# Optimization experiments

Measured on AMD Instinct MI355X. Metric: run time of the kernel, lower is better.

The kernel has to match this reference:

```python
import jax, jax.numpy as jnp
import numpy as np

B = 4096
M = 4            # n_modalities
T = 8            # n_tasks
D = 1024         # feature_dim per modality
DIN = D * M      # concat feature dim = 4096
H = 256          # hidden_dim
H2 = 2 * H       # 512
TEMP = 1.0
EPS = 1e-5


def _layernorm(x, g, b):
    # LayerNorm over last axis (torch nn.LayerNorm semantics, eps=1e-5)
    mu = jnp.mean(x, axis=-1, keepdims=True)
    var = jnp.mean(jnp.square(x - mu), axis=-1, keepdims=True)
    return (x - mu) * jax.lax.rsqrt(var + EPS) * g + b


def setup_inputs() -> dict:
    key = jax.random.key(0)
    ks = jax.random.split(key, 16)
    s = 0.02
    return {
        "f0": jax.random.normal(ks[0], (B, D), jnp.float32),
        "f1": jax.random.normal(ks[1], (B, D), jnp.float32),
        "f2": jax.random.normal(ks[2], (B, D), jnp.float32),
        "f3": jax.random.normal(ks[3], (B, D), jnp.float32),
        # per-task feature-net params (stacked ModuleList)
        "W1": jax.random.normal(ks[4], (T, DIN, H2), jnp.float32) * s,
        "b1": jnp.zeros((T, H2), jnp.float32),
        "g1": jnp.ones((T, H2), jnp.float32),
        "be1": jnp.zeros((T, H2), jnp.float32),
        "W2": jax.random.normal(ks[5], (T, H2, H), jnp.float32) * s,
        "b2": jnp.zeros((T, H), jnp.float32),
        "g2": jnp.ones((T, H), jnp.float32),
        "be2": jnp.zeros((T, H), jnp.float32),
        "task_emb": jax.random.normal(ks[6], (T, H), jnp.float32),
        # per-task weight-net params (Linear(2H -> M))
        "Ww": jax.random.normal(ks[7], (T, H2, M), jnp.float32) * s,
        "bw": jnp.zeros((T, M), jnp.float32),
        "task_ids": jax.random.randint(ks[8], (B,), 0, T, jnp.int32),
    }


def reference(f0, f1, f2, f3, W1, b1, g1, be1, W2, b2, g2, be2, task_emb, Ww, bw, task_ids):
    x = jnp.concatenate([f0, f1, f2, f3], axis=1)              # [B, DIN]
    # compute all-task feature nets densely (T is small), then gather per sample
    h = jnp.einsum('bd,tdh->bth', x, W1) + b1[None]            # [B, T, 2H]
    h = jax.nn.relu(_layernorm(h, g1[None], be1[None]))
    h = jnp.einsum('bth,thk->btk', h, W2) + b2[None]           # [B, T, H]
    h = jax.nn.relu(_layernorm(h, g2[None], be2[None]))
    hid = jnp.take_along_axis(h, task_ids[:, None, None], axis=1)[:, 0]  # [B, H]
    te = task_emb[task_ids]                                    # [B, H]
    comb = jnp.concatenate([hid, te], axis=1)                  # [B, 2H]
    # per-sample gather of small weight-net matrices (irregular access)
    raw = jnp.einsum('bh,bhm->bm', comb, Ww[task_ids]) + bw[task_ids]    # [B, M]
    return jax.nn.softmax(raw / TEMP, axis=1)
```

## Files before the change

kernel.cpp:

```cpp
#include <hip/hip_runtime.h>
#include <stdint.h>

#define B_N 4096
#define T_N 8
#define DIN 4096
#define H2C 512
#define HC 256
#define NWG1 1024
#define NWG2 264
#define SPLITK1 4

typedef __attribute__((ext_vector_type(8))) short bf16x8;
typedef __attribute__((ext_vector_type(4))) float f32x4;

static __device__ __forceinline__ unsigned short f2bf(float f) {
    union { float f; uint32_t u; } v; v.f = f;
    uint32_t u = v.u;
    uint32_t r = (u + 0x7FFFu + ((u >> 16) & 1u)) >> 16;
    return (unsigned short)r;
}

static __device__ __forceinline__ float bf2f(uint32_t h) {
    union { uint32_t u; float f; } v; v.u = h << 16; return v.f;
}

static __device__ __forceinline__ uint32_t pk2(float a, float b) {
    uint32_t r;
    asm volatile("v_cvt_pk_bf16_f32 %0, %1, %2" : "=v"(r) : "v"(a), "v"(b));
    return r;
}

static __device__ __forceinline__ void gl2lds16(const unsigned short* g, unsigned short* l) {
    __builtin_amdgcn_global_load_lds(
        (const __attribute__((address_space(1))) unsigned int*)(g),
        (__attribute__((address_space(3))) unsigned int*)(l), 16, 0, 0);
}

static __device__ __forceinline__ int xcd_remap(int bid, int nwg) {
    int xcd = bid & 7, idx = bid >> 3;
    int q = nwg >> 3, r = nwg & 7;
    return (xcd < r ? xcd * (q + 1) : r * (q + 1) + (xcd - r) * q) + idx;
}

__launch_bounds__(256)
__global__ void k_pre(const float* __restrict__ W1, const float* __restrict__ W2,
                      const int* __restrict__ task_ids,
                      const float* __restrict__ temb, const float* __restrict__ Ww,
                      const float* __restrict__ bw,
                      unsigned short* __restrict__ W1t, unsigned short* __restrict__ W2t,
                      int* __restrict__ order, int* __restrict__ tiles, int* __restrict__ bmap,
                      int* __restrict__ tiles2, int* __restrict__ ntile2,
                      float* __restrict__ tb) {
    int blk = blockIdx.x, tid = threadIdx.x;
    if (blk == 0) {
        __shared__ unsigned long long wtot[4][2];
        __shared__ int lc[T_N], lseg[T_N], tb1p[T_N + 1], tb2p[T_N + 1];
        int lane = tid & 63, wv = tid >> 6;
        int4 a0 = *(const int4*)(task_ids + tid * 16);
        int4 a1 = *(const int4*)(task_ids + tid * 16 + 4);
        int4 a2 = *(const int4*)(task_ids + tid * 16 + 8);
        int4 a3 = *(const int4*)(task_ids + tid * 16 + 12);
        int myt[16] = {a0.x, a0.y, a0.z, a0.w, a1.x, a1.y, a1.z, a1.w,
                       a2.x, a2.y, a2.z, a2.w, a3.x, a3.y, a3.z, a3.w};
        unsigned long long ph0 = 0, ph1 = 0;
        #pragma unroll
        for (int i = 0; i < 16; ++i) {
            int t = myt[i];
            if (t < 4) ph0 += 1ull << (t * 16); else ph1 += 1ull << ((t - 4) * 16);
        }
        unsigned long long s0 = ph0, s1 = ph1;
        for (int o = 1; o < 64; o <<= 1) {
            unsigned long long u0 = __shfl_up(s0, o);
            unsigned long long u1 = __shfl_up(s1, o);
            if (lane >= o) { s0 += u0; s1 += u1; }
        }
        if (lane == 63) { wtot[wv][0] = s0; wtot[wv][1] = s1; }
        __syncthreads();
        unsigned long long e0 = s0 - ph0, e1 = s1 - ph1;
        for (int w2 = 0; w2 < wv; ++w2) { e0 += wtot[w2][0]; e1 += wtot[w2][1]; }
        if (tid == 0) {
            unsigned long long t0 = 0, t1 = 0;
            for (int w2 = 0; w2 < 4; ++w2) { t0 += wtot[w2][0]; t1 += wtot[w2][1]; }
            int s = 0;
            for (int t = 0; t < T_N; ++t) {
                int c = (int)((t < 4 ? (t0 >> (t * 16)) : (t1 >> ((t - 4) * 16))) & 0xFFFF);
                lc[t] = c; lseg[t] = s; s += c;
            }
            int q1 = 0, q2 = 0;
            for (int t = 0; t < T_N; ++t) {
                tb1p[t] = q1; tb2p[t] = q2;
                q1 += (lc[t] + 127) >> 7; q2 += (lc[t] + 15) >> 4;
            }
            tb1p[T_N] = q1; tb2p[T_N] = q2;
            ntile2[0] = q2;
        }
        __syncthreads();
        unsigned long long r0 = e0, r1 = e1;
        #pragma unroll
        for (int i = 0; i < 16; ++i) {
            int t = myt[i], rk;
            if (t < 4) { rk = (int)((r0 >> (t * 16)) & 0xFFFF); r0 += 1ull << (t * 16); }
            else { int u = t - 4; rk = (int)((r1 >> (u * 16)) & 0xFFFF); r1 += 1ull << (u * 16); }
            order[lseg[t] + rk] = tid * 16 + i;
        }
        int n1 = tb1p[T_N], n2 = tb2p[T_N];
        for (int e = tid; e < n1; e += 256) {
            int t = 0; while (e >= tb1p[t + 1]) ++t;
            int rr = (e - tb1p[t]) << 7;
            tiles[3 * e] = t; tiles[3 * e + 1] = lseg[t] + rr;
            int rem = lc[t] - rr; tiles[3 * e + 2] = rem < 128 ? rem : 128;
        }
        for (int e = tid; e < n2; e += 256) {
            int t = 0; while (e >= tb2p[t + 1]) ++t;
            int rr = (e - tb2p[t]) << 4;
            tiles2[3 * e] = t; tiles2[3 * e + 1] = lseg[t] + rr;
            int rem = lc[t] - rr; tiles2[3 * e + 2] = rem < 16 ? rem : 16;
        }
        for (int s = tid; s < NWG1; s += 256) {
            int t = s & 7, j = s >> 3;
            int base = tb1p[t], nt = tb1p[t + 1] - base;
            bmap[s] = (j < nt * 16) ? (((base + (j >> 4)) << 4) | (j & 15)) : -1;
        }
        __syncthreads();
        if (tid == 0) {
            int freeslot = 0;
            for (int t = 0; t < T_N; ++t) {
                int base = tb1p[t], nt = tb1p[t + 1] - base;
                for (int j = 128; j < nt * 16; ++j) {
                    while (bmap[freeslot] >= 0) ++freeslot;
                    bmap[freeslot] = ((base + (j >> 4)) << 4) | (j & 15);
                }
            }
        }
        for (int t = wv; t < T_N; t += 4) {
            int m = lane & 3, hb = (lane >> 2) * 16;
            float s = 0.f;
            for (int h = 0; h < 16; ++h)
                s += temb[t * HC + hb + h] * Ww[((size_t)t * H2C + HC + hb + h) * 4 + m];
            for (int o = 4; o < 64; o <<= 1) s += __shfl_xor(s, o);
            if (lane < 4) tb[t * 4 + lane] = s + bw[t * 4 + lane];
        }
        return;
    }
    __shared__ float tile[64][65];
    const float* ip; unsigned short* op; int R, C, bx, by, t;
    if (blk < 4097) {
        int idx = blk - 1; bx = idx & 63; by = (idx >> 6) & 7; t = idx >> 9;
        R = DIN; C = H2C;
        ip = W1 + (size_t)t * R * C; op = W1t + (size_t)t * R * C;
    } else {
        int idx = blk - 4097; bx = idx & 7; by = (idx >> 3) & 3; t = idx >> 5;
        R = H2C; C = HC;
        ip = W2 + (size_t)t * R * C; op = W2t + (size_t)t * R * C;
    }
    int r0 = bx * 64, c0 = by * 64;
    int lr = tid >> 4, lc4 = (tid & 15) * 4;
    #pragma unroll
    for (int i = 0; i < 4; ++i) {
        float4 v = *(const float4*)&ip[(size_t)(r0 + lr + i * 16) * C + c0 + lc4];
        tile[lr + i * 16][lc4 + 0] = v.x;
        tile[lr + i * 16][lc4 + 1] = v.y;
        tile[lr + i * 16][lc4 + 2] = v.z;
        tile[lr + i * 16][lc4 + 3] = v.w;
    }
    __syncthreads();
    int r4 = (tid & 15) * 4;
    #pragma unroll
    for (int i = 0; i < 4; ++i) {
        int cc = i * 16 + (tid >> 4);
        uint2 wv;
        wv.x = (uint32_t)f2bf(tile[r4 + 0][cc]) | ((uint32_t)f2bf(tile[r4 + 1][cc]) << 16);
        wv.y = (uint32_t)f2bf(tile[r4 + 2][cc]) | ((uint32_t)f2bf(tile[r4 + 3][cc]) << 16);
        *(uint2*)&op[(size_t)(c0 + cc) * R + r0 + r4] = wv;
    }
}

__launch_bounds__(256)
__global__ void k_gemm1(const float* __restrict__ f0, const float* __restrict__ f1,
                        const float* __restrict__ f2, const float* __restrict__ f3,
                        const unsigned short* __restrict__ Bt,
                        unsigned short* __restrict__ Cb16, const int* __restrict__ order,
                        const int* __restrict__ tiles, const int* __restrict__ bmap) {
    int e = bmap[blockIdx.x];
    if (e < 0) return;
    int tix = e >> 4, sub = e & 15;
    int ct = sub >> 2, kc = sub & 3;
    int t = tiles[3 * tix], prow = tiles[3 * tix + 1], rows = tiles[3 * tix + 2];
    int kb = kc * (DIN / SPLITK1);
    const float* fsrc = (kc == 0) ? f0 : (kc == 1) ? f1 : (kc == 2) ? f2 : f3;

    __shared__ unsigned short lds[2][16384];

    int tid = threadIdx.x, lane = tid & 63, w = tid >> 6;
    int wm = w >> 1, wn = w & 1;

    const float* srcA[4];
    int ldsA[4];
    #pragma unroll
    for (int i = 0; i < 4; ++i) {
        int gi = i * 256 + tid;
        int row = gi >> 3, g = gi & 7;
        int rl = row < rows ? row : rows - 1;
        srcA[i] = fsrc + (size_t)order[prow + rl] * 1024 + g * 8;
        ldsA[i] = row * 64 + ((g ^ (row & 7)) * 8);
    }
    const unsigned short* pB[4];
    #pragma unroll
    for (int j = 0; j < 4; ++j) {
        int row = j * 32 + (tid >> 3);
        int colg = (tid & 7) ^ (row & 7);
        pB[j] = Bt + ((size_t)t * H2C + ct * 128 + row) * DIN + kb + colg * 8;
    }

    float4 a0[4], a1[4];
    auto loadA = [&](int k0) {
        #pragma unroll
        for (int i = 0; i < 4; ++i) {
            a0[i] = *(const float4*)(srcA[i] + k0);
            a1[i] = *(const float4*)(srcA[i] + k0 + 4);
        }
    };
    auto writeA = [&](int buf) {
        #pragma unroll
        for (int i = 0; i < 4; ++i) {
            uint4 wv;
            wv.x = pk2(a0[i].x, a0[i].y); wv.y = pk2(a0[i].z, a0[i].w);
            wv.z = pk2(a1[i].x, a1[i].y); wv.w = pk2(a1[i].z, a1[i].w);
            *(uint4*)&lds[buf][ldsA[i]] = wv;
        }
    };
    auto stageB = [&](int buf, int it) {
        unsigned short* dB = &lds[buf][8192 + w * 512];
        #pragma unroll
        for (int j = 0; j < 4; ++j) gl2lds16(pB[j] + it * 64, dB + j * 2048);
    };

    f32x4 acc[4][4];
    #pragma unroll
    for (int m = 0; m < 4; ++m)
        #pragma unroll
        for (int n = 0; n < 4; ++n)
            acc[m][n] = (f32x4){0.f, 0.f, 0.f, 0.f};

    constexpr int NIT = DIN / SPLITK1 / 64;
    loadA(0);
    stageB(0, 0);
    writeA(0);
    __syncthreads();
    int cur = 0;
    for (int it = 0; it < NIT; ++it) {
        if (it + 1 < NIT) {
            loadA((it + 1) * 64);
            stageB(cur ^ 1, it + 1);
            __builtin_amdgcn_sched_barrier(0);
        }
        const unsigned short* As = &lds[cur][0];
        const unsigned short* Bs = As + 8192;
        #pragma unroll
        for (int ks = 0; ks < 2; ++ks) {
            int g = ks * 4 + (lane >> 4);
            bf16x8 af[4], bfv[4];
            #pragma unroll
            for (int m = 0; m < 4; ++m) {
                int row = wm * 64 + m * 16 + (lane & 15);
                af[m] = *(const bf16x8*)&As[row * 64 + ((g ^ (row & 7)) * 8)];
            }
            #pragma unroll
            for (int n = 0; n < 4; ++n) {
                int row = wn * 64 + n * 16 + (lane & 15);
                bfv[n] = *(const bf16x8*)&Bs[row * 64 + ((g ^ (row & 7)) * 8)];
            }
            #pragma unroll
            for (int m = 0; m < 4; ++m)
                #pragma unroll
                for (int n = 0; n < 4; ++n)
                    acc[m][n] = __builtin_amdgcn_mfma_f32_16x16x32_bf16(af[m], bfv[n], acc[m][n], 0, 0, 0);
        }
        if (it + 1 < NIT) writeA(cur ^ 1);
        __syncthreads();
        cur ^= 1;
    }

    unsigned short* Cb = Cb16 + (size_t)kc * B_N * H2C;
    #pragma unroll
    for (int m = 0; m < 4; ++m) {
        #pragma unroll
        for (int n = 0; n < 4; ++n) {
            int col = ct * 128 + wn * 64 + n * 16 + (lane & 15);
            #pragma unroll
            for (int j = 0; j < 4; ++j) {
                int row = wm * 64 + m * 16 + (lane >> 4) * 4 + j;
                if (row < rows)
                    Cb[(size_t)(prow + row) * H2C + col] = f2bf(acc[m][n][j]);
            }
        }
    }
}

__launch_bounds__(256)
__global__ void k_gemm2f(const unsigned short* __restrict__ h1p, const unsigned short* __restrict__ W2t,
                         const float* __restrict__ b1, const float* __restrict__ g1,
                         const float* __restrict__ be1,
                         const float* __restrict__ b2, const float* __restrict__ g2,
                         const float* __restrict__ be2,
                         const float* __restrict__ Ww, const float* __restrict__ tb,
                         const int* __restrict__ order,
                         const int* __restrict__ tiles2, const int* __restrict__ ntile2,
                         float* __restrict__ out) {
    __shared__ unsigned short Asm[16 * 512];
    __shared__ unsigned short Bsm[2][256 * 32];
    __shared__ float red[16][4][4];

    int id = xcd_remap(blockIdx.x, NWG2);
    if (id >= ntile2[0]) return;
    int t = tiles2[3 * id], prow = tiles2[3 * id + 1], rows = tiles2[3 * id + 2];
    int tid = threadIdx.x, lane = tid & 63, w = tid >> 6;

    {
        int r = tid >> 4;
        int rl = r < rows ? r : rows - 1;
        int c0 = (tid & 15) * 32;
        const unsigned short* p0 = h1p + (size_t)(prow + rl) * H2C + c0;
        const float* pb = b1 + t * H2C + c0;
        float x[32];
        float s = 0.f, sq = 0.f;
        #pragma unroll
        for (int i = 0; i < 32; i += 8) {
            uint4 u0 = *(const uint4*)(p0 + i);
            uint4 u1 = *(const uint4*)(p0 + (size_t)B_N * H2C + i);
            uint4 u2 = *(const uint4*)(p0 + (size_t)2 * B_N * H2C + i);
            uint4 u3 = *(const uint4*)(p0 + (size_t)3 * B_N * H2C + i);
            uint32_t w0[4] = {u0.x, u0.y, u0.z, u0.w};
            uint32_t w1[4] = {u1.x, u1.y, u1.z, u1.w};
            uint32_t w2[4] = {u2.x, u2.y, u2.z, u2.w};
            uint32_t w3[4] = {u3.x, u3.y, u3.z, u3.w};
            float4 c0v = *(const float4*)(pb + i);
            float4 c1v = *(const float4*)(pb + i + 4);
            float cv[8] = {c0v.x, c0v.y, c0v.z, c0v.w, c1v.x, c1v.y, c1v.z, c1v.w};
            #pragma unroll
            for (int q = 0; q < 4; ++q) {
                float v0 = bf2f(w0[q] & 0xFFFFu) + bf2f(w1[q] & 0xFFFFu)
                         + bf2f(w2[q] & 0xFFFFu) + bf2f(w3[q] & 0xFFFFu) + cv[2 * q];
                float v1 = bf2f(w0[q] >> 16) + bf2f(w1[q] >> 16)
                         + bf2f(w2[q] >> 16) + bf2f(w3[q] >> 16) + cv[2 * q + 1];
                x[i + 2 * q] = v0; x[i + 2 * q + 1] = v1;
                s += v0 + v1; sq += v0 * v0 + v1 * v1;
            }
        }
        #pragma unroll
        for (int o = 1; o < 16; o <<= 1) { s += __shfl_xor(s, o); sq += __shfl_xor(sq, o); }
        float mean = s * (1.f / H2C);
        float var = sq * (1.f / H2C) - mean * mean;
        float rstd = rsqrtf(var + 1e-5f);
        const float* pg = g1 + t * H2C + c0;
        const float* pe = be1 + t * H2C + c0;
        #pragma unroll
        for (int i = 0; i < 32; i += 8) {
            unsigned short y[8];
            #pragma unroll
            for (int q = 0; q < 8; q += 4) {
                float4 gv = *(const float4*)(pg + i + q);
                float4 ev = *(const float4*)(pe + i + q);
                y[q + 0] = f2bf(fmaxf((x[i + q + 0] - mean) * rstd * gv.x + ev.x, 0.f));
                y[q + 1] = f2bf(fmaxf((x[i + q + 1] - mean) * rstd * gv.y + ev.y, 0.f));
                y[q + 2] = f2bf(fmaxf((x[i + q + 2] - mean) * rstd * gv.z + ev.z, 0.f));
                y[q + 3] = f2bf(fmaxf((x[i + q + 3] - mean) * rstd * gv.w + ev.w, 0.f));
            }
            uint4 wv;
            wv.x = (uint32_t)y[0] | ((uint32_t)y[1] << 16);
            wv.y = (uint32_t)y[2] | ((uint32_t)y[3] << 16);
            wv.z = (uint32_t)y[4] | ((uint32_t)y[5] << 16);
            wv.w = (uint32_t)y[6] | ((uint32_t)y[7] << 16);
            int g = (c0 + i) >> 3;
            *(uint4*)&Asm[r * 512 + ((g ^ (r & 7)) * 8)] = wv;
        }
    }

    auto stageB = [&](int buf, int it) {
        #pragma unroll
        for (int j = 0; j < 4; ++j) {
            int G = j * 256 + tid;
            int row = G >> 2, g = G & 3;
            int colg = g ^ (row & 3);
            gl2lds16(W2t + ((size_t)t * HC + row) * H2C + it * 32 + colg * 8,
                     &Bsm[buf][(j * 256 + w * 64) * 8]);
        }
    };

    stageB(0, 0);
    __syncthreads();

    f32x4 acc[4];
    #pragma unroll
    for (int n = 0; n < 4; ++n) acc[n] = (f32x4){0.f, 0.f, 0.f, 0.f};

    for (int it = 0; it < 16; ++it) {
        if (it + 1 < 16) stageB((it + 1) & 1, it + 1);
        const unsigned short* Bs = &Bsm[it & 1][0];
        int g = lane >> 4;
        int arow = lane & 15;
        bf16x8 af = *(const bf16x8*)&Asm[arow * 512 + (((it * 4 + g) ^ (arow & 7)) * 8)];
        #pragma unroll
        for (int n = 0; n < 4; ++n) {
            int brow = w * 64 + n * 16 + arow;
            bf16x8 bv = *(const bf16x8*)&Bs[brow * 32 + ((g ^ (brow & 3)) * 8)];
            acc[n] = __builtin_amdgcn_mfma_f32_16x16x32_bf16(af, bv, acc[n], 0, 0, 0);
        }
        __syncthreads();
    }

    float b2v[4], g2v[4], e2v[4];
    float4 wv[4];
    #pragma unroll
    for (int n = 0; n < 4; ++n) {
        int col = w * 64 + n * 16 + (lane & 15);
        b2v[n] = b2[t * HC + col];
        g2v[n] = g2[t * HC + col];
        e2v[n] = be2[t * HC + col];
        wv[n] = *(const float4*)&Ww[((size_t)t * H2C + col) * 4];
    }
    float s4[4], q4[4];
    #pragma unroll
    for (int j = 0; j < 4; ++j) {
        float s = 0.f, sq = 0.f;
        #pragma unroll
        for (int n = 0; n < 4; ++n) {
            float xv = acc[n][j] + b2v[n];
            s += xv; sq += xv * xv;
        }
        #pragma unroll
        for (int o = 1; o < 16; o <<= 1) { s += __shfl_xor(s, o); sq += __shfl_xor(sq, o); }
        s4[j] = s; q4[j] = sq;
    }
    if ((lane & 15) == 0) {
        #pragma unroll
        for (int j = 0; j < 4; ++j) {
            int r = (lane >> 4) * 4 + j;
            red[r][w][0] = s4[j];
            red[r][w][1] = q4[j];
        }
    }
    __syncthreads();
    float mean[4], rstd[4];
    #pragma unroll
    for (int j = 0; j < 4; ++j) {
        int r = (lane >> 4) * 4 + j;
        float S = red[r][0][0] + red[r][1][0] + red[r][2][0] + red[r][3][0];
        float SQ = red[r][0][1] + red[r][1][1] + red[r][2][1] + red[r][3][1];
        mean[j] = S * (1.f / HC);
        float var = SQ * (1.f / HC) - mean[j] * mean[j];
        rstd[j] = rsqrtf(var + 1e-5f);
    }
    float p[4][4];
    #pragma unroll
    for (int j = 0; j < 4; ++j) {
        p[j][0] = 0.f; p[j][1] = 0.f; p[j][2] = 0.f; p[j][3] = 0.f;
        #pragma unroll
        for (int n = 0; n < 4; ++n) {
            float yv = fmaxf((acc[n][j] + b2v[n] - mean[j]) * rstd[j] * g2v[n] + e2v[n], 0.f);
            p[j][0] += yv * wv[n].x; p[j][1] += yv * wv[n].y;
            p[j][2] += yv * wv[n].z; p[j][3] += yv * wv[n].w;
        }
        #pragma unroll
        for (int m = 0; m < 4; ++m)
            #pragma unroll
            for (int o = 1; o < 16; o <<= 1) p[j][m] += __shfl_xor(p[j][m], o);
    }
    __syncthreads();
    if ((lane & 15) == 0) {
        #pragma unroll
        for (int j = 0; j < 4; ++j) {
            int r = (lane >> 4) * 4 + j;
            red[r][w][0] = p[j][0]; red[r][w][1] = p[j][1];
            red[r][w][2] = p[j][2]; red[r][w][3] = p[j][3];
        }
    }
    __syncthreads();
    if (tid < 16 && tid < rows) {
        float raw[4];
        #pragma unroll
        for (int m = 0; m < 4; ++m)
            raw[m] = red[tid][0][m] + red[tid][1][m] + red[tid][2][m] + red[tid][3][m] + tb[t * 4 + m];
        float mx = fmaxf(fmaxf(raw[0], raw[1]), fmaxf(raw[2], raw[3]));
        float e0 = expf(raw[0] - mx), e1 = expf(raw[1] - mx);
        float e2 = expf(raw[2] - mx), e3 = expf(raw[3] - mx);
        float si = 1.f / (e0 + e1 + e2 + e3);
        *(float4*)(out + (size_t)order[prow + tid] * 4) = make_float4(e0 * si, e1 * si, e2 * si, e3 * si);
    }
}

extern "C" void kernel_launch(void* const* d_in, const int* in_sizes, int n_in,
                              void* d_out, int out_size, void* d_ws, size_t ws_size,
                              hipStream_t stream) {
    const float* f0 = (const float*)d_in[0];
    const float* f1 = (const float*)d_in[1];
    const float* f2 = (const float*)d_in[2];
    const float* f3 = (const float*)d_in[3];
    const float* W1 = (const float*)d_in[4];
    const float* b1 = (const float*)d_in[5];
    const float* g1 = (const float*)d_in[6];
    const float* be1 = (const float*)d_in[7];
    const float* W2 = (const float*)d_in[8];
    const float* b2 = (const float*)d_in[9];
    const float* g2 = (const float*)d_in[10];
    const float* be2 = (const float*)d_in[11];
    const float* temb = (const float*)d_in[12];
    const float* Ww = (const float*)d_in[13];
    const float* bw = (const float*)d_in[14];
    const int* task_ids = (const int*)d_in[15];
    float* out = (float*)d_out;

    char* ws = (char*)d_ws;
    size_t off = 0;
    auto walloc = [&](size_t bytes) -> void* {
        void* p = ws + off;
        off = (off + bytes + 255) & ~(size_t)255;
        return p;
    };
    float* tb = (float*)walloc(128);
    int* tiles = (int*)walloc(64 * 3 * 4);
    int* bmap = (int*)walloc(NWG1 * 4);
    int* tiles2 = (int*)walloc(272 * 3 * 4);
    int* ntile2 = (int*)walloc(4);
    int* order = (int*)walloc((size_t)B_N * 4);
    unsigned short* W1t = (unsigned short*)walloc((size_t)T_N * H2C * DIN * 2);
    unsigned short* W2t = (unsigned short*)walloc((size_t)T_N * HC * H2C * 2);
    unsigned short* h1p = (unsigned short*)walloc((size_t)SPLITK1 * B_N * H2C * 2);

    k_pre<<<4353, 256, 0, stream>>>(W1, W2, task_ids, temb, Ww, bw,
                                    W1t, W2t, order, tiles, bmap, tiles2, ntile2, tb);
    k_gemm1<<<NWG1, 256, 0, stream>>>(f0, f1, f2, f3, W1t, h1p, order, tiles, bmap);
    k_gemm2f<<<NWG2, 256, 0, stream>>>(h1p, W2t, b1, g1, be1, b2, g2, be2, Ww, tb,
                                       order, tiles2, ntile2, out);
}
```

Measured before the change: 81.88 us.

## Stage fp32 activations directly to LDS via global_load_lds and convert at fragment load

In the first GEMM, the A operand (fp32 features) is no longer loaded into registers, converted to bf16 and written to LDS. It is now copied asynchronously into LDS as fp32 with global_load_lds and converted to bf16 when each MFMA fragment is read. The K step per iteration is halved from 64 to 32, and the B tile uses a new XOR swizzle to match. This removes the register round-trip and VGPR pressure of the A path. In exchange it doubles A's LDS footprint per element, adds conversion work inside the MFMA loop, and doubles the number of barriers.

```diff
diff --git a/kernel.cpp b/kernel.cpp
--- a/kernel.cpp
+++ b/kernel.cpp
@@ -31,6 +31,12 @@
 }
 
 static __device__ __forceinline__ void gl2lds16(const unsigned short* g, unsigned short* l) {
+    __builtin_amdgcn_global_load_lds(
+        (const __attribute__((address_space(1))) unsigned int*)(g),
+        (__attribute__((address_space(3))) unsigned int*)(l), 16, 0, 0);
+}
+
+static __device__ __forceinline__ void gl2lds16f(const float* g, float* l) {
     __builtin_amdgcn_global_load_lds(
         (const __attribute__((address_space(1))) unsigned int*)(g),
         (__attribute__((address_space(3))) unsigned int*)(l), 16, 0, 0);
@@ -189,50 +195,35 @@
     int kb = kc * (DIN / SPLITK1);
     const float* fsrc = (kc == 0) ? f0 : (kc == 1) ? f1 : (kc == 2) ? f2 : f3;
 
-    __shared__ unsigned short lds[2][16384];
+    __shared__ float ldsA[2][128 * 32];
+    __shared__ unsigned short ldsB[2][128 * 32];
 
     int tid = threadIdx.x, lane = tid & 63, w = tid >> 6;
     int wm = w >> 1, wn = w & 1;
 
-    const float* srcA[4];
-    int ldsA[4];
-    #pragma unroll
-    for (int i = 0; i < 4; ++i) {
-        int gi = i * 256 + tid;
-        int row = gi >> 3, g = gi & 7;
+    const float* pA4[4];
+    #pragma unroll
+    for (int j = 0; j < 4; ++j) {
+        int slot = j * 256 + tid;
+        int row = slot >> 3, gd = slot & 7;
         int rl = row < rows ? row : rows - 1;
-        srcA[i] = fsrc + (size_t)order[prow + rl] * 1024 + g * 8;
-        ldsA[i] = row * 64 + ((g ^ (row & 7)) * 8);
-    }
-    const unsigned short* pB[4];
-    #pragma unroll
-    for (int j = 0; j < 4; ++j) {
-        int row = j * 32 + (tid >> 3);
-        int colg = (tid & 7) ^ (row & 7);
-        pB[j] = Bt + ((size_t)t * H2C + ct * 128 + row) * DIN + kb + colg * 8;
-    }
-
-    float4 a0[4], a1[4];
-    auto loadA = [&](int k0) {
-        #pragma unroll
-        for (int i = 0; i < 4; ++i) {
-            a0[i] = *(const float4*)(srcA[i] + k0);
-            a1[i] = *(const float4*)(srcA[i] + k0 + 4);
-        }
-    };
-    auto writeA = [&](int buf) {
-        #pragma unroll
-        for (int i = 0; i < 4; ++i) {
-            uint4 wv;
-            wv.x = pk2(a0[i].x, a0[i].y); wv.y = pk2(a0[i].z, a0[i].w);
-            wv.z = pk2(a1[i].x, a1[i].y); wv.w = pk2(a1[i].z, a1[i].w);
-            *(uint4*)&lds[buf][ldsA[i]] = wv;
-        }
-    };
-    auto stageB = [&](int buf, int it) {
-        unsigned short* dB = &lds[buf][8192 + w * 512];
-        #pragma unroll
-        for (int j = 0; j < 4; ++j) gl2lds16(pB[j] + it * 64, dB + j * 2048);
+        pA4[j] = fsrc + (size_t)order[prow + rl] * 1024 + (gd ^ (row & 7)) * 4;
+    }
+    const unsigned short* pB[2];
+    #pragma unroll
+    for (int j = 0; j < 2; ++j) {
+        int slot = j * 256 + tid;
+        int row = slot >> 2, gd = slot & 3;
+        pB[j] = Bt + ((size_t)t * H2C + ct * 128 + row) * DIN + kb + (gd ^ ((row >> 1) & 3)) * 8;
+    }
+
+    auto stage = [&](int buf, int it) {
+        float* dA = &ldsA[buf][(size_t)w * 256];
+        unsigned short* dB = &ldsB[buf][(size_t)w * 512];
+        #pragma unroll
+        for (int j = 0; j < 4; ++j) gl2lds16f(pA4[j] + it * 32, dA + j * 1024);
+        #pragma unroll
+        for (int j = 0; j < 2; ++j) gl2lds16(pB[j] + it * 32, dB + j * 2048);
     };
 
     f32x4 acc[4][4];
@@ -242,41 +233,36 @@
         for (int n = 0; n < 4; ++n)
             acc[m][n] = (f32x4){0.f, 0.f, 0.f, 0.f};
 
-    constexpr int NIT = DIN / SPLITK1 / 64;
-    loadA(0);
-    stageB(0, 0);
-    writeA(0);
+    constexpr int NIT = (DIN / SPLITK1) / 32;
+    stage(0, 0);
     __syncthreads();
     int cur = 0;
+    int g = lane >> 4, lrow = lane & 15;
     for (int it = 0; it < NIT; ++it) {
-        if (it + 1 < NIT) {
-            loadA((it + 1) * 64);
-            stageB(cur ^ 1, it + 1);
-            __builtin_amdgcn_sched_barrier(0);
-        }
-        const unsigned short* As = &lds[cur][0];
-        const unsigned short* Bs = As + 8192;
-        #pragma unroll
-        for (int ks = 0; ks < 2; ++ks) {
-            int g = ks * 4 + (lane >> 4);
-            bf16x8 af[4], bfv[4];
+        if (it + 1 < NIT) stage(cur ^ 1, it + 1);
+        const float* Af = &ldsA[cur][0];
+        const unsigned short* Bs = &ldsB[cur][0];
+        bf16x8 af[4], bfv[4];
+        #pragma unroll
+        for (int m = 0; m < 4; ++m) {
+            int row = wm * 64 + m * 16 + lrow;
+            float4 lo = *(const float4*)(Af + row * 32 + (((2 * g) ^ (row & 7)) * 4));
+            float4 hi = *(const float4*)(Af + row * 32 + (((2 * g + 1) ^ (row & 7)) * 4));
+            union { uint4 u; bf16x8 b; } cv;
+            cv.u.x = pk2(lo.x, lo.y); cv.u.y = pk2(lo.z, lo.w);
+            cv.u.z = pk2(hi.x, hi.y); cv.u.w = pk2(hi.z, hi.w);
+            af[m] = cv.b;
+        }
+        #pragma unroll
+        for (int n = 0; n < 4; ++n) {
+            int row = wn * 64 + n * 16 + lrow;
+            bfv[n] = *(const bf16x8*)&Bs[row * 32 + ((g ^ ((row >> 1) & 3)) * 8)];
+        }
+        #pragma unroll
+        for (int m = 0; m < 4; ++m)
             #pragma unroll
-            for (int m = 0; m < 4; ++m) {
-                int row = wm * 64 + m * 16 + (lane & 15);
-                af[m] = *(const bf16x8*)&As[row * 64 + ((g ^ (row & 7)) * 8)];
-            }
-            #pragma unroll
-            for (int n = 0; n < 4; ++n) {
-                int row = wn * 64 + n * 16 + (lane & 15);
-                bfv[n] = *(const bf16x8*)&Bs[row * 64 + ((g ^ (row & 7)) * 8)];
-            }
-            #pragma unroll
-            for (int m = 0; m < 4; ++m)
-                #pragma unroll
-                for (int n = 0; n < 4; ++n)
-                    acc[m][n] = __builtin_amdgcn_mfma_f32_16x16x32_bf16(af[m], bfv[n], acc[m][n], 0, 0, 0);
-        }
-        if (it + 1 < NIT) writeA(cur ^ 1);
+            for (int n = 0; n < 4; ++n)
+                acc[m][n] = __builtin_amdgcn_mfma_f32_16x16x32_bf16(af[m], bfv[n], acc[m][n], 0, 0, 0);
         __syncthreads();
         cur ^= 1;
     }
```

After: 85.04 us. +3.9%, slower.

## Deepen A-operand prefetch to two stages with explicit vmcnt waits

Applied to the files above, without the earlier changes.

Adds a second register set for the fp32 A tile so global loads are issued two iterations ahead instead of one. Replaces __syncthreads with hand-placed s_waitcnt vmcnt/lgkmcnt counts plus s_barrier, so outstanding B direct-to-LDS loads and A loads can overlap the MFMA work. This hides more global memory latency at the cost of extra VGPRs (32 more floats per thread), which may lower occupancy. The hardcoded wait counts depend on the exact load-issue order, so any mismatch could cause hazards.

```diff
diff --git a/kernel.cpp b/kernel.cpp
--- a/kernel.cpp
+++ b/kernel.cpp
@@ -212,20 +212,20 @@
         pB[j] = Bt + ((size_t)t * H2C + ct * 128 + row) * DIN + kb + colg * 8;
     }
 
-    float4 a0[4], a1[4];
-    auto loadA = [&](int k0) {
+    float4 a0[2][4], a1[2][4];
+    auto loadA = [&](int set, int k0) {
         #pragma unroll
         for (int i = 0; i < 4; ++i) {
-            a0[i] = *(const float4*)(srcA[i] + k0);
-            a1[i] = *(const float4*)(srcA[i] + k0 + 4);
+            a0[set][i] = *(const float4*)(srcA[i] + k0);
+            a1[set][i] = *(const float4*)(srcA[i] + k0 + 4);
         }
     };
-    auto writeA = [&](int buf) {
+    auto writeA = [&](int buf, int set) {
         #pragma unroll
         for (int i = 0; i < 4; ++i) {
             uint4 wv;
-            wv.x = pk2(a0[i].x, a0[i].y); wv.y = pk2(a0[i].z, a0[i].w);
-            wv.z = pk2(a1[i].x, a1[i].y); wv.w = pk2(a1[i].z, a1[i].w);
+            wv.x = pk2(a0[set][i].x, a0[set][i].y); wv.y = pk2(a0[set][i].z, a0[set][i].w);
+            wv.z = pk2(a1[set][i].x, a1[set][i].y); wv.w = pk2(a1[set][i].z, a1[set][i].w);
             *(uint4*)&lds[buf][ldsA[i]] = wv;
         }
     };
@@ -242,18 +242,19 @@
         for (int n = 0; n < 4; ++n)
             acc[m][n] = (f32x4){0.f, 0.f, 0.f, 0.f};
 
-    constexpr int NIT = DIN / SPLITK1 / 64;
-    loadA(0);
+    constexpr int NIT = 16;
+    loadA(0, 0);
     stageB(0, 0);
-    writeA(0);
-    __syncthreads();
+    writeA(0, 0);
+    loadA(1, 64);
+    __builtin_amdgcn_sched_barrier(0);
+    asm volatile("s_waitcnt vmcnt(8) lgkmcnt(0)" ::: "memory");
+    __builtin_amdgcn_sched_barrier(0);
+    __builtin_amdgcn_s_barrier();
+
     int cur = 0;
     for (int it = 0; it < NIT; ++it) {
-        if (it + 1 < NIT) {
-            loadA((it + 1) * 64);
-            stageB(cur ^ 1, it + 1);
-            __builtin_amdgcn_sched_barrier(0);
-        }
+        if (it + 1 < NIT) stageB(cur ^ 1, it + 1);
         const unsigned short* As = &lds[cur][0];
         const unsigned short* Bs = As + 8192;
         #pragma unroll
@@ -276,8 +277,20 @@
                 for (int n = 0; n < 4; ++n)
                     acc[m][n] = __builtin_amdgcn_mfma_f32_16x16x32_bf16(af[m], bfv[n], acc[m][n], 0, 0, 0);
         }
-        if (it + 1 < NIT) writeA(cur ^ 1);
-        __syncthreads();
+        if (it + 1 < NIT) {
+            asm volatile("s_waitcnt vmcnt(4)" ::: "memory");
+            __builtin_amdgcn_sched_barrier(0);
+            writeA(cur ^ 1, (it + 1) & 1);
+            if (it + 2 < NIT) {
+                loadA((it + 2) & 1, (it + 2) * 64);
+                __builtin_amdgcn_sched_barrier(0);
+                asm volatile("s_waitcnt vmcnt(8) lgkmcnt(0)" ::: "memory");
+            } else {
+                asm volatile("s_waitcnt vmcnt(0) lgkmcnt(0)" ::: "memory");
+            }
+            __builtin_amdgcn_sched_barrier(0);
+            __builtin_amdgcn_s_barrier();
+        }
         cur ^= 1;
     }
 
```

After: 216.4 us. 2.64x slower.
